# Performance work log

Hardware: AMD Instinct MI355X
Metric: run time of the kernel (lower is better)

## Reference

```python
import jax, jax.numpy as jnp
import numpy as np

B, C, H, W = 4, 256, 64, 64
NH, NQ, HD, WS = 4, 16, 64, 3   # num_heads, num_queries, head_dim, attn_window_size
PD = NH * HD                    # proj_dim = 256


def setup_inputs() -> dict:
    key = jax.random.key(0)
    ks = jax.random.split(key, 6)
    s = 0.02
    return {
        "x": jax.random.normal(ks[0], (B, C, H, W), jnp.float32),
        "kv_w": jax.random.normal(ks[1], (2 * PD, C), jnp.float32) * s,
        "dot_w": jax.random.normal(ks[2], (NH, NQ, HD), jnp.float32) * s,
        "head_w": jax.random.normal(ks[3], (HD, PD), jnp.float32) * s,
        "head_b": jnp.zeros((HD,), jnp.float32),
        "q_w": jax.random.normal(ks[4], (C, NQ * HD), jnp.float32) * s,
        "q_b": jnp.zeros((C,), jnp.float32),
    }


def _unfold(x, ws):
    """Sliding ws x ws patches over last two dims (stride 1, same padding).
    x: (..., h, w) -> (..., h, w, ws*ws), flattened in (i*ws + j) order
    matching torch's unfold(2).unfold(3)."""
    pad = ws // 2
    padw = [(0, 0)] * (x.ndim - 2) + [(pad, pad), (pad, pad)]
    xp = jnp.pad(x, padw)
    h, w = x.shape[-2], x.shape[-1]
    return jnp.stack(
        [xp[..., i:i + h, j:j + w] for i in range(ws) for j in range(ws)],
        axis=-1,
    )


def reference(x, kv_w, dot_w, head_w, head_b, q_w, q_b):
    b, c, h, w = x.shape
    # kv 1x1 conv, then split into k, v (each proj_dim channels)
    kv = jnp.einsum('oc,bchw->bohw', kv_w, x)
    k, v = jnp.split(kv, 2, axis=1)
    # grouped 1x1 conv: per-head head_dim -> num_queries (NOTE: no scale; the
    # original defines self.scale but never applies it in forward)
    kh = k.reshape(b, NH, HD, h, w)
    attn = jnp.einsum('bndhw,nqd->bnqhw', kh, dot_w)
    # unfold overlapping 3x3 windows (L = ws^2 = 9)
    attn_p = _unfold(attn, WS)                        # (b, n, q, h, w, L)
    v_p = _unfold(v.reshape(b, NH, HD, h, w), WS)     # (b, n, d, h, w, L)
    attn_p = jax.nn.softmax(attn_p, axis=-1)
    # per-pixel weighted sum over the window, arranged as (b, q, n, d, h, w)
    out = jnp.einsum('bnqhwl,bndhwl->bqndhw', attn_p, v_p)
    out = out.reshape(b, NQ, PD, h, w)                # (n d) -> proj_dim channels
    # head_proj: 1x1 conv proj_dim -> head_dim (dropout=0)
    y = jnp.einsum('op,bqphw->bqohw', head_w, out) + head_b[None, None, :, None, None]
    # query_proj: 1x1 conv (k*head_dim) -> dim (dropout=0)
    y = y.reshape(b, NQ * HD, h, w)
    z = jnp.einsum('oc,bchw->bohw', q_w, y) + q_b[None, :, None, None]
    return z
```

## Files before the change

kernel.cpp:

```cpp
#include <hip/hip_runtime.h>
#include <hip/hip_bf16.h>
#include <cstdint>

typedef __hip_bfloat16 bf16;
using bf16x8 = __attribute__((ext_vector_type(8))) short;
using f32x4  = __attribute__((ext_vector_type(4))) float;

#define HW_T 4096
#define B_T  4

__device__ __forceinline__ void async_copy16(const bf16* g, bf16* l) {
    __builtin_amdgcn_global_load_lds(
        (const __attribute__((address_space(1))) void*)g,
        (__attribute__((address_space(3))) void*)l, 16, 0, 0);
}
__device__ __forceinline__ short f2bs(float f) {
    bf16 h = __float2bfloat16(f);
    return *reinterpret_cast<short*>(&h);
}
__device__ __forceinline__ float bs2f(short s) {
    unsigned int u = ((unsigned int)(unsigned short)s) << 16;
    float f;
    __builtin_memcpy(&f, &u, 4);
    return f;
}

__global__ __launch_bounds__(256) void fuse_all(
    const float* __restrict__ kv_w, const float* __restrict__ dot_w,
    const float* __restrict__ head_w, const float* __restrict__ q_w,
    bf16* __restrict__ W, bf16* __restrict__ qwF)
{
    const int rb = blockIdx.x;
    if (rb < 384) {
        const int r = rb, c = threadIdx.x;
        float acc = 0.f;
        if (r < 64) {
            const int n = r >> 4, q = r & 15;
            #pragma unroll 8
            for (int d = 0; d < 64; ++d)
                acc += dot_w[(n * 16 + q) * 64 + d] * kv_w[(size_t)(n * 64 + d) * 256 + c];
        } else if (r < 320) {
            const int rr = r - 64, n = rr >> 6, dh = rr & 63;
            #pragma unroll 8
            for (int dd = 0; dd < 64; ++dd)
                acc += head_w[dh * 256 + n * 64 + dd] * kv_w[(size_t)(256 + n * 64 + dd) * 256 + c];
        }
        W[r * 256 + c] = __float2bfloat16(acc);
    } else {
        const int t  = (rb - 384) * 256 + threadIdx.x;
        const int ch = t & 255, kb = t >> 8;
        const float* src = q_w + (size_t)ch * 1024 + kb * 8;
        bf16x8 pk;
        #pragma unroll
        for (int j = 0; j < 8; ++j) pk[j] = f2bs(src[j]);
        *(bf16x8*)&qwF[(size_t)t * 8] = pk;
    }
}

__global__ __launch_bounds__(256) void gemm_xw(
    const float* __restrict__ x, const bf16* __restrict__ W,
    bf16* __restrict__ AH)
{
    __shared__ __align__(16) bf16 As[2][4][32][8];
    __shared__ __align__(16) bf16 Bs[2][4][384][8];
    const int tid  = threadIdx.x;
    const int wave = tid >> 6, lane = tid & 63;
    const int p0 = blockIdx.x * 32;
    const int b  = blockIdx.y;
    const float* xb = x + (size_t)b * 256 * HW_T;
    const int fi = lane & 15, quad = lane >> 4;
    const int wn0 = wave * 96;

    const int apx = tid & 31, ac8 = (tid >> 5) & 3;
    const bool aStage = tid < 128;

    f32x4 acc[2][6] = {};
    float xr[8];

    #pragma unroll
    for (int i = 0; i < 6; ++i) {
        const int s = i * 256 + tid;
        const int ch = s % 384, q = s / 384;
        async_copy16(W + (size_t)ch * 256 + q * 8,
                     &Bs[0][0][0][0] + (size_t)(i * 256 + wave * 64) * 8);
    }
    if (aStage) {
        const float* xp = xb + (size_t)(ac8 * 8) * HW_T + p0 + apx;
        #pragma unroll
        for (int j = 0; j < 8; ++j) xr[j] = xp[(size_t)j * HW_T];
        bf16x8 pk;
        #pragma unroll
        for (int j = 0; j < 8; ++j) pk[j] = f2bs(xr[j]);
        *(bf16x8*)&As[0][ac8][apx][0] = pk;
    }

    for (int it = 0; it < 8; ++it) {
        const int cur = it & 1;
        __syncthreads();
        if (it < 7) {
            const int k1 = (it + 1) * 32;
            #pragma unroll
            for (int i = 0; i < 6; ++i) {
                const int s = i * 256 + tid;
                const int ch = s % 384, q = s / 384;
                async_copy16(W + (size_t)ch * 256 + k1 + q * 8,
                             &Bs[cur ^ 1][0][0][0] + (size_t)(i * 256 + wave * 64) * 8);
            }
            if (aStage) {
                const float* xp = xb + (size_t)(k1 + ac8 * 8) * HW_T + p0 + apx;
                #pragma unroll
                for (int j = 0; j < 8; ++j) xr[j] = xp[(size_t)j * HW_T];
            }
        }
        bf16x8 af[2], bfr[6];
        #pragma unroll
        for (int i = 0; i < 2; ++i)
            af[i] = *(const bf16x8*)&As[cur][quad][i * 16 + fi][0];
        #pragma unroll
        for (int j = 0; j < 6; ++j)
            bfr[j] = *(const bf16x8*)&Bs[cur][quad][wn0 + j * 16 + fi][0];
        #pragma unroll
        for (int i = 0; i < 2; ++i)
            #pragma unroll
            for (int j = 0; j < 6; ++j)
                acc[i][j] = __builtin_amdgcn_mfma_f32_16x16x32_bf16(
                    af[i], bfr[j], acc[i][j], 0, 0, 0);
        if (it < 7 && aStage) {
            bf16x8 pk;
            #pragma unroll
            for (int j = 0; j < 8; ++j) pk[j] = f2bs(xr[j]);
            *(bf16x8*)&As[cur ^ 1][ac8][apx][0] = pk;
        }
    }

    bf16* Cp = AH + ((size_t)b * HW_T + p0) * 384;
    #pragma unroll
    for (int i = 0; i < 2; ++i) {
        const int pl = i * 16 + quad * 4;
        #pragma unroll
        for (int r = 0; r < 4; ++r)
            #pragma unroll
            for (int j = 0; j < 6; ++j)
                Cp[(size_t)(pl + r) * 384 + wn0 + j * 16 + fi] =
                    __float2bfloat16(acc[i][j][r]);
    }
}

#define YPAD 1032
#define ATTN_LDS (64 * YPAD * 2 + 8 * 9 * 64 * 4)

__global__ __launch_bounds__(512) void attn_qy(
    const bf16* __restrict__ AH, const float* __restrict__ head_b,
    const bf16* __restrict__ qwF, const float* __restrict__ q_b,
    float* __restrict__ z)
{
    extern __shared__ __align__(16) char smem[];
    bf16*  yL = (bf16*)smem;
    float* Pm = (float*)(smem + 64 * YPAD * 2) + (threadIdx.x >> 6) * 9 * 64;

    const int tid  = threadIdx.x;
    const int wave = tid >> 6, lane = tid & 63;
    const int p0  = blockIdx.x * 64;
    const int b   = p0 >> 12;
    const int hw0 = p0 & 4095;
    const int h   = hw0 >> 6;
    const int fi = lane & 15, quad = lane >> 4;
    const ushort* AHu = (const ushort*)AH;

    float hb[4];
    #pragma unroll
    for (int dt = 0; dt < 4; ++dt) hb[dt] = head_b[dt * 16 + fi];

    for (int pi = 0; pi < 8; ++pi) {
        const int w = wave * 8 + pi;
        int off[9]; float okf[9];
        #pragma unroll
        for (int l = 0; l < 9; ++l) {
            const int i = l / 3, j = l % 3;
            const int hh = h + i - 1, ww = w + j - 1;
            const bool ok = ((unsigned)hh < 64u) && ((unsigned)ww < 64u);
            off[l] = ((b << 12) + (ok ? hh : h) * 64 + (ok ? ww : w)) * 384;
            okf[l] = ok ? 1.0f : 0.0f;
        }
        {
            float lg[9];
            #pragma unroll
            for (int l = 0; l < 9; ++l)
                lg[l] = bs2f((short)AHu[(size_t)off[l] + lane]) * okf[l];
            float m = lg[0];
            #pragma unroll
            for (int l = 1; l < 9; ++l) m = fmaxf(m, lg[l]);
            float e[9], s = 0.f;
            #pragma unroll
            for (int l = 0; l < 9; ++l) { e[l] = __expf(lg[l] - m); s += e[l]; }
            const float inv = 1.0f / s;
            #pragma unroll
            for (int l = 0; l < 9; ++l) Pm[l * 64 + lane] = e[l] * inv * okf[l];
        }

        bf16x8 afr;
        #pragma unroll
        for (int j = 0; j < 8; ++j) {
            const int k = quad * 8 + j;
            afr[j] = f2bs(Pm[(k >> 2) * 64 + (k & 3) * 16 + fi]);
        }
        f32x4 acc[4];
        #pragma unroll
        for (int dt = 0; dt < 4; ++dt) {
            acc[dt][0] = hb[dt]; acc[dt][1] = hb[dt];
            acc[dt][2] = hb[dt]; acc[dt][3] = hb[dt];
        }
        #pragma unroll
        for (int dt = 0; dt < 4; ++dt) {
            bf16x8 bfr;
            #pragma unroll
            for (int j = 0; j < 8; ++j) {
                const int k = quad * 8 + j;
                bfr[j] = (short)AHu[(size_t)off[k >> 2] + 64 + (k & 3) * 64 + dt * 16 + fi];
            }
            acc[dt] = __builtin_amdgcn_mfma_f32_16x16x32_bf16(afr, bfr, acc[dt], 0, 0, 0);
        }
        #pragma unroll
        for (int n = 0; n < 4; ++n) {
            float pv[4];
            #pragma unroll
            for (int r = 0; r < 4; ++r) pv[r] = Pm[8 * 64 + n * 16 + quad * 4 + r];
            #pragma unroll
            for (int dt = 0; dt < 4; ++dt) {
                const float hval =
                    bs2f((short)AHu[(size_t)off[8] + 64 + n * 64 + dt * 16 + fi]);
                #pragma unroll
                for (int r = 0; r < 4; ++r) acc[dt][r] = fmaf(pv[r], hval, acc[dt][r]);
            }
        }
        #pragma unroll
        for (int dt = 0; dt < 4; ++dt)
            #pragma unroll
            for (int r = 0; r < 4; ++r)
                yL[(size_t)w * YPAD + (quad * 4 + r) * 64 + dt * 16 + fi] =
                    __float2bfloat16(acc[dt][r]);
    }
    __syncthreads();

    f32x4 zacc[2][4] = {};
    bf16x8 af[2], afn[2];
    #pragma unroll
    for (int i = 0; i < 2; ++i)
        af[i] = *(const bf16x8*)&qwF[((size_t)quad * 256 + wave * 32 + i * 16 + fi) * 8];

    #pragma unroll 2
    for (int k0 = 0; k0 < 1024; k0 += 32) {
        if (k0 < 992) {
            const size_t kb = (size_t)((k0 + 32) >> 3) + quad;
            #pragma unroll
            for (int i = 0; i < 2; ++i)
                afn[i] = *(const bf16x8*)&qwF[(kb * 256 + wave * 32 + i * 16 + fi) * 8];
        }
        bf16x8 bfr[4];
        #pragma unroll
        for (int j = 0; j < 4; ++j)
            bfr[j] = *(const bf16x8*)&yL[(size_t)(j * 16 + fi) * YPAD + k0 + quad * 8];
        #pragma unroll
        for (int i = 0; i < 2; ++i)
            #pragma unroll
            for (int j = 0; j < 4; ++j)
                zacc[i][j] = __builtin_amdgcn_mfma_f32_16x16x32_bf16(
                    af[i], bfr[j], zacc[i][j], 0, 0, 0);
        af[0] = afn[0]; af[1] = afn[1];
    }

    #pragma unroll
    for (int i = 0; i < 2; ++i) {
        const int row0 = wave * 32 + i * 16 + quad * 4;
        #pragma unroll
        for (int r = 0; r < 4; ++r) {
            const float bv = q_b[row0 + r];
            #pragma unroll
            for (int j = 0; j < 4; ++j)
                z[((size_t)(b * 256 + row0 + r)) * HW_T + hw0 + j * 16 + fi] =
                    zacc[i][j][r] + bv;
        }
    }
}

extern "C" void kernel_launch(void* const* d_in, const int* in_sizes, int n_in,
                              void* d_out, int out_size, void* d_ws, size_t ws_size,
                              hipStream_t stream) {
    (void)in_sizes; (void)n_in; (void)out_size; (void)ws_size;
    const float* x      = (const float*)d_in[0];
    const float* kv_w   = (const float*)d_in[1];
    const float* dot_w  = (const float*)d_in[2];
    const float* head_w = (const float*)d_in[3];
    const float* head_b = (const float*)d_in[4];
    const float* q_w    = (const float*)d_in[5];
    const float* q_b    = (const float*)d_in[6];
    float* z = (float*)d_out;

    char* ws   = (char*)d_ws;
    bf16*  AH  = (bf16*)ws;
    bf16*  W   = (bf16*)(ws + 12582912);
    bf16*  qwF = (bf16*)(ws + 12779520);

    static bool attr_done = []() {
        hipFuncSetAttribute((const void*)attn_qy,
                            hipFuncAttributeMaxDynamicSharedMemorySize, ATTN_LDS);
        return true;
    }();
    (void)attr_done;

    fuse_all<<<dim3(512), 256, 0, stream>>>(kv_w, dot_w, head_w, q_w, W, qwF);

    gemm_xw<<<dim3(128, B_T), 256, 0, stream>>>(x, W, AH);

    attn_qy<<<dim3(256), 512, ATTN_LDS, stream>>>(AH, head_b, qwF, q_b, z);
}
```

Measured before the change: 131.8 us.

## Drop unused padding rows and load pre-swizzled weights directly into registers

The fused weight matrix is trimmed from 384 to 320 rows, dropping 64 rows that were always zero. This shrinks the intermediate AH buffer and the GEMM's N dimension. The weights are now written in a k-block-major layout so each wave reads its MFMA B fragments straight from global memory into registers, with a register double buffer replacing the LDS staging. The A-tile staging is spread across all 256 threads instead of 128. A __syncthreads is added in attn_qy after the softmax probabilities are written to LDS; since Pm is per-wave, this barrier adds synchronisation that was not needed before.

Measured after the change: 121.2 us. 8.1% less time.

```diff
diff --git a/kernel.cpp b/kernel.cpp
--- a/kernel.cpp
+++ b/kernel.cpp
@@ -9,11 +9,6 @@
 #define HW_T 4096
 #define B_T  4
 
-__device__ __forceinline__ void async_copy16(const bf16* g, bf16* l) {
-    __builtin_amdgcn_global_load_lds(
-        (const __attribute__((address_space(1))) void*)g,
-        (__attribute__((address_space(3))) void*)l, 16, 0, 0);
-}
 __device__ __forceinline__ short f2bs(float f) {
     bf16 h = __float2bfloat16(f);
     return *reinterpret_cast<short*>(&h);
@@ -28,10 +23,10 @@
 __global__ __launch_bounds__(256) void fuse_all(
     const float* __restrict__ kv_w, const float* __restrict__ dot_w,
     const float* __restrict__ head_w, const float* __restrict__ q_w,
-    bf16* __restrict__ W, bf16* __restrict__ qwF)
+    bf16* __restrict__ Wf, bf16* __restrict__ qwF)
 {
     const int rb = blockIdx.x;
-    if (rb < 384) {
+    if (rb < 320) {
         const int r = rb, c = threadIdx.x;
         float acc = 0.f;
         if (r < 64) {
@@ -39,15 +34,15 @@
             #pragma unroll 8
             for (int d = 0; d < 64; ++d)
                 acc += dot_w[(n * 16 + q) * 64 + d] * kv_w[(size_t)(n * 64 + d) * 256 + c];
-        } else if (r < 320) {
+        } else {
             const int rr = r - 64, n = rr >> 6, dh = rr & 63;
             #pragma unroll 8
             for (int dd = 0; dd < 64; ++dd)
                 acc += head_w[dh * 256 + n * 64 + dd] * kv_w[(size_t)(256 + n * 64 + dd) * 256 + c];
         }
-        W[r * 256 + c] = __float2bfloat16(acc);
+        Wf[((size_t)(c >> 3) * 320 + r) * 8 + (c & 7)] = __float2bfloat16(acc);
     } else {
-        const int t  = (rb - 384) * 256 + threadIdx.x;
+        const int t  = (rb - 320) * 256 + threadIdx.x;
         const int ch = t & 255, kb = t >> 8;
         const float* src = q_w + (size_t)ch * 1024 + kb * 8;
         bf16x8 pk;
@@ -58,40 +53,35 @@
 }
 
 __global__ __launch_bounds__(256) void gemm_xw(
-    const float* __restrict__ x, const bf16* __restrict__ W,
+    const float* __restrict__ x, const bf16* __restrict__ Wf,
     bf16* __restrict__ AH)
 {
     __shared__ __align__(16) bf16 As[2][4][32][8];
-    __shared__ __align__(16) bf16 Bs[2][4][384][8];
     const int tid  = threadIdx.x;
-    const int wave = tid >> 6, lane = tid & 63;
+    const int lane = tid & 63;
+    const int wave = tid >> 6;
     const int p0 = blockIdx.x * 32;
     const int b  = blockIdx.y;
     const float* xb = x + (size_t)b * 256 * HW_T;
     const int fi = lane & 15, quad = lane >> 4;
-    const int wn0 = wave * 96;
-
-    const int apx = tid & 31, ac8 = (tid >> 5) & 3;
-    const bool aStage = tid < 128;
-
-    f32x4 acc[2][6] = {};
-    float xr[8];
-
-    #pragma unroll
-    for (int i = 0; i < 6; ++i) {
-        const int s = i * 256 + tid;
-        const int ch = s % 384, q = s / 384;
-        async_copy16(W + (size_t)ch * 256 + q * 8,
-                     &Bs[0][0][0][0] + (size_t)(i * 256 + wave * 64) * 8);
-    }
-    if (aStage) {
-        const float* xp = xb + (size_t)(ac8 * 8) * HW_T + p0 + apx;
-        #pragma unroll
-        for (int j = 0; j < 8; ++j) xr[j] = xp[(size_t)j * HW_T];
-        bf16x8 pk;
-        #pragma unroll
-        for (int j = 0; j < 8; ++j) pk[j] = f2bs(xr[j]);
-        *(bf16x8*)&As[0][ac8][apx][0] = pk;
+    const int wn0 = wave * 80;
+
+    const int spx = tid & 31, sk = (tid >> 5) * 4;
+
+    f32x4 acc[2][5] = {};
+    float xr[4];
+    bf16x8 bcur[5], bnxt[5];
+
+    {
+        const float* xp = xb + (size_t)sk * HW_T + p0 + spx;
+        #pragma unroll
+        for (int j = 0; j < 4; ++j) xr[j] = xp[(size_t)j * HW_T];
+        #pragma unroll
+        for (int j = 0; j < 5; ++j)
+            bcur[j] = *(const bf16x8*)&Wf[((size_t)quad * 320 + wn0 + j * 16 + fi) * 8];
+        short4 pk;
+        pk.x = f2bs(xr[0]); pk.y = f2bs(xr[1]); pk.z = f2bs(xr[2]); pk.w = f2bs(xr[3]);
+        *(short4*)&As[0][sk >> 3][spx][sk & 7] = pk;
     }
 
     for (int it = 0; it < 8; ++it) {
@@ -99,49 +89,42 @@
         __syncthreads();
         if (it < 7) {
             const int k1 = (it + 1) * 32;
-            #pragma unroll
-            for (int i = 0; i < 6; ++i) {
-                const int s = i * 256 + tid;
-                const int ch = s % 384, q = s / 384;
-                async_copy16(W + (size_t)ch * 256 + k1 + q * 8,
-                             &Bs[cur ^ 1][0][0][0] + (size_t)(i * 256 + wave * 64) * 8);
-            }
-            if (aStage) {
-                const float* xp = xb + (size_t)(k1 + ac8 * 8) * HW_T + p0 + apx;
-                #pragma unroll
-                for (int j = 0; j < 8; ++j) xr[j] = xp[(size_t)j * HW_T];
-            }
-        }
-        bf16x8 af[2], bfr[6];
+            const float* xp = xb + (size_t)(k1 + sk) * HW_T + p0 + spx;
+            #pragma unroll
+            for (int j = 0; j < 4; ++j) xr[j] = xp[(size_t)j * HW_T];
+            const size_t kb = (size_t)(k1 >> 3) + quad;
+            #pragma unroll
+            for (int j = 0; j < 5; ++j)
+                bnxt[j] = *(const bf16x8*)&Wf[(kb * 320 + wn0 + j * 16 + fi) * 8];
+        }
+        bf16x8 af[2];
         #pragma unroll
         for (int i = 0; i < 2; ++i)
             af[i] = *(const bf16x8*)&As[cur][quad][i * 16 + fi][0];
         #pragma unroll
-        for (int j = 0; j < 6; ++j)
-            bfr[j] = *(const bf16x8*)&Bs[cur][quad][wn0 + j * 16 + fi][0];
-        #pragma unroll
         for (int i = 0; i < 2; ++i)
             #pragma unroll
-            for (int j = 0; j < 6; ++j)
+            for (int j = 0; j < 5; ++j)
                 acc[i][j] = __builtin_amdgcn_mfma_f32_16x16x32_bf16(
-                    af[i], bfr[j], acc[i][j], 0, 0, 0);
-        if (it < 7 && aStage) {
-            bf16x8 pk;
-            #pragma unroll
-            for (int j = 0; j < 8; ++j) pk[j] = f2bs(xr[j]);
-            *(bf16x8*)&As[cur ^ 1][ac8][apx][0] = pk;
-        }
-    }
-
-    bf16* Cp = AH + ((size_t)b * HW_T + p0) * 384;
+                    af[i], bcur[j], acc[i][j], 0, 0, 0);
+        if (it < 7) {
+            short4 pk;
+            pk.x = f2bs(xr[0]); pk.y = f2bs(xr[1]); pk.z = f2bs(xr[2]); pk.w = f2bs(xr[3]);
+            *(short4*)&As[cur ^ 1][sk >> 3][spx][sk & 7] = pk;
+            #pragma unroll
+            for (int j = 0; j < 5; ++j) bcur[j] = bnxt[j];
+        }
+    }
+
+    bf16* Cp = AH + ((size_t)b * HW_T + p0) * 320;
     #pragma unroll
     for (int i = 0; i < 2; ++i) {
         const int pl = i * 16 + quad * 4;
         #pragma unroll
         for (int r = 0; r < 4; ++r)
             #pragma unroll
-            for (int j = 0; j < 6; ++j)
-                Cp[(size_t)(pl + r) * 384 + wn0 + j * 16 + fi] =
+            for (int j = 0; j < 5; ++j)
+                Cp[(size_t)(pl + r) * 320 + wn0 + j * 16 + fi] =
                     __float2bfloat16(acc[i][j][r]);
     }
 }
@@ -179,7 +162,7 @@
             const int i = l / 3, j = l % 3;
             const int hh = h + i - 1, ww = w + j - 1;
             const bool ok = ((unsigned)hh < 64u) && ((unsigned)ww < 64u);
-            off[l] = ((b << 12) + (ok ? hh : h) * 64 + (ok ? ww : w)) * 384;
+            off[l] = ((b << 12) + (ok ? hh : h) * 64 + (ok ? ww : w)) * 320;
             okf[l] = ok ? 1.0f : 0.0f;
         }
         {
@@ -197,6 +180,7 @@
             #pragma unroll
             for (int l = 0; l < 9; ++l) Pm[l * 64 + lane] = e[l] * inv * okf[l];
         }
+        __syncthreads();
 
         bf16x8 afr;
         #pragma unroll
@@ -298,8 +282,8 @@
 
     char* ws   = (char*)d_ws;
     bf16*  AH  = (bf16*)ws;
-    bf16*  W   = (bf16*)(ws + 12582912);
-    bf16*  qwF = (bf16*)(ws + 12779520);
+    bf16*  qwF = (bf16*)(ws + 10485760);
+    bf16*  Wf  = (bf16*)(ws + 11010048);
 
     static bool attr_done = []() {
         hipFuncSetAttribute((const void*)attn_qy,
@@ -308,9 +292,9 @@
     }();
     (void)attr_done;
 
-    fuse_all<<<dim3(512), 256, 0, stream>>>(kv_w, dot_w, head_w, q_w, W, qwF);
-
-    gemm_xw<<<dim3(128, B_T), 256, 0, stream>>>(x, W, AH);
+    fuse_all<<<dim3(448), 256, 0, stream>>>(kv_w, dot_w, head_w, q_w, Wf, qwF);
+
+    gemm_xw<<<dim3(128, B_T), 256, 0, stream>>>(x, Wf, AH);
 
     attn_qy<<<dim3(256), 512, ATTN_LDS, stream>>>(AH, head_b, qwF, q_b, z);
 }
```
